# Kernel tuning notes

Measured on AMD Instinct MI355X. Metric: run time of the kernel, lower is better.

Reference implementation:

```python
import jax, jax.numpy as jnp
import numpy as np

# Dimensions (match init_kwargs / input_specs)
B, C, H, W = 16, 96, 224, 224
COUT = 96
PH, PW = 16, 16          # patch_size (== patch_stride, non-overlapping)
KH, KW = 3, 3            # patch_kernel and output_kernel
PAD = 1                  # padding
GH, GW = H // PH, W // PW
P = GH * GW              # num_patches = 196


def setup_inputs() -> dict:
    key = jax.random.key(0)
    k1, k2, k3 = jax.random.split(key, 3)
    x = jax.random.normal(k1, (B, C, H, W), dtype=jnp.float32)
    # kaiming-normal-ish init scales (fan_in over trailing dims, as torch does)
    pf = jax.random.normal(k2, (C, P, 1, KH, KW), dtype=jnp.float32) * np.float32(np.sqrt(2.0 / (P * KH * KW)))
    of = jax.random.normal(k3, (COUT, C, KH, KW), dtype=jnp.float32) * np.float32(np.sqrt(2.0 / (C * KH * KW)))
    return {"x": x, "patch_filters": pf, "output_filters": of}


def _self_conv2d(x, patch_filters):
    """Locally-connected per-patch depthwise conv.

    x: (B, C, H, W); patch_filters: (C, P, 1, KH, KW).
    Each of the P non-overlapping PHxPW patches of each channel is convolved
    with its own KHxKW kernel (padding=PAD, stride=1), then patches are
    reassembled into the full (B, C, H, W) map.
    """
    # (B, C, GH, PH, GW, PW) -> (B, C, GH, GW, PH, PW) -> (B, C*P, PH, PW)
    xp = x.reshape(B, C, GH, PH, GW, PW).transpose(0, 1, 2, 4, 3, 5).reshape(B, C * P, PH, PW)
    k = patch_filters.reshape(C * P, 1, KH, KW)
    y = jax.lax.conv_general_dilated(
        xp, k,
        window_strides=(1, 1),
        padding=[(PAD, PAD), (PAD, PAD)],
        feature_group_count=C * P,
        dimension_numbers=("NCHW", "OIHW", "NCHW"),
    )  # (B, C*P, PH, PW) since 3x3 conv with pad 1 preserves size
    return y.reshape(B, C, GH, GW, PH, PW).transpose(0, 1, 2, 4, 3, 5).reshape(B, C, H, W)


def reference(x, patch_filters, output_filters):
    # input already at (max_input_height, max_input_width) -> F.pad is a no-op
    sa = _self_conv2d(x, patch_filters)
    out = jax.lax.conv_general_dilated(
        sa, output_filters,
        window_strides=(1, 1),
        padding=[(PAD, PAD), (PAD, PAD)],
        dimension_numbers=("NCHW", "OIHW", "NCHW"),
    )  # (B, COUT, H, W)
    return jax.nn.gelu(out, approximate=False)  # torch nn.GELU() = exact erf gelu
```

## Files before the change

kernel.cpp:

```cpp
#include <hip/hip_runtime.h>
#include <hip/hip_bf16.h>

#define B_    16
#define C_    96
#define H_    224
#define W_    224
#define COUT_ 96
#define GH_   14
#define GW_   14
#define P_    196
#define HW_   (H_*W_)
#define NCH_  12

#define AS1 __attribute__((address_space(1)))
#define AS3 __attribute__((address_space(3)))

typedef __attribute__((ext_vector_type(8))) unsigned short ushort8;
typedef __attribute__((ext_vector_type(8))) short        short8;
typedef __attribute__((ext_vector_type(4))) float        f32x4;

__device__ __forceinline__ unsigned short f2bf(float f) {
    union { __hip_bfloat16 h; unsigned short u; } cv;
    cv.h = __float2bfloat16(f);
    return cv.u;
}

__global__ __launch_bounds__(256) void prep_ofb(const float* __restrict__ of,
                                                unsigned short* __restrict__ ofb3,
                                                unsigned short* __restrict__ zp) {
    if (blockIdx.x == 0 && threadIdx.x < 128) zp[threadIdx.x] = 0;
    int e = blockIdx.x * 256 + threadIdx.x;
    if (e < 82944) {
        int j    = e & 7;
        int l    = (e >> 3) & 63;
        int ni   = (e >> 9) % 6;
        int cs   = (e / 3072) % 3;
        int tap  = e / 9216;
        int cout = ni * 16 + (l & 15);
        int c    = cs * 32 + (l >> 4) * 8 + j;
        ofb3[e] = f2bf(of[((size_t)cout * 96 + c) * 9 + tap]);
    }
}

__global__ __launch_bounds__(256) void sa_kernel(const float* __restrict__ x,
                                                 const float* __restrict__ pf,
                                                 unsigned short* __restrict__ sa) {
    int bid   = blockIdx.x;
    int patch = bid % P_;
    int b     = bid / P_;
    int gh = patch / GW_, gw = patch % GW_;
    int t  = threadIdx.x;
    int py = t >> 4, px = t & 15;
    int y  = gh * 16 + py, xx = gw * 16 + px;

    __shared__ float xs[2][8][256];

    const float* xp0 = x + (size_t)b * C_ * HW_ + (size_t)y * W_ + xx;

    float lf[8];
    #pragma unroll
    for (int ch = 0; ch < 8; ++ch) lf[ch] = xp0[(size_t)ch * HW_];

    for (int cc = 0; cc < NCH_; ++cc) {
        int buf = cc & 1;
        #pragma unroll
        for (int ch = 0; ch < 8; ++ch) xs[buf][ch][t] = lf[ch];
        __syncthreads();
        if (cc < NCH_ - 1) {
            #pragma unroll
            for (int ch = 0; ch < 8; ++ch)
                lf[ch] = xp0[(size_t)((cc + 1) * 8 + ch) * HW_];
        }

        ushort8 v;
        #pragma unroll
        for (int ch = 0; ch < 8; ++ch) {
            const float* wgt = pf + ((size_t)(cc * 8 + ch) * P_ + patch) * 9;
            float a = 0.f;
            #pragma unroll
            for (int dy = -1; dy <= 1; ++dy) {
                int yy = py + dy;
                if ((unsigned)yy < 16u) {
                    #pragma unroll
                    for (int dx = -1; dx <= 1; ++dx) {
                        int xq = px + dx;
                        if ((unsigned)xq < 16u)
                            a = fmaf(xs[buf][ch][yy * 16 + xq],
                                     wgt[(dy + 1) * 3 + (dx + 1)], a);
                    }
                }
            }
            v[ch] = f2bf(a);
        }
        *(ushort8*)&sa[(((size_t)(b * NCH_ + cc) * H_ + y) * W_ + xx) * 8] = v;
    }
}

__global__ __launch_bounds__(256, 3) void conv2_mfma(const unsigned short* __restrict__ sa,
                                                     const unsigned short* __restrict__ ofb3,
                                                     const unsigned short* __restrict__ zp,
                                                     float* __restrict__ out) {
    int bid0 = blockIdx.x;
    int bid  = (bid0 % 8) * (6272 / 8) + bid0 / 8;
    int half = bid & 1;
    int pid  = bid >> 1;
    int patch = pid % P_;
    int b     = pid / P_;
    int gh = patch / GW_, gw = patch % GW_;
    int y0 = gh * 16 + half * 8, x0 = gw * 16;

    int t = threadIdx.x;
    int w = t >> 6, l = t & 63;
    int wm = w & 1, wn = w >> 1;
    int mrow = l & 15, kgrp = l >> 4;

    __shared__ ushort8 at8[2304];

    #pragma unroll
    for (int i = 0; i < 9; ++i) {
        int v = t + i * 256;
        const unsigned short* src = zp;
        if (v < 2160) {
            int ccl = v / 180, hpx = v - ccl * 180;
            int gy = y0 - 1 + hpx / 18, gx = x0 - 1 + hpx % 18;
            if ((unsigned)gy < (unsigned)H_ && (unsigned)gx < (unsigned)W_)
                src = &sa[(((size_t)(b * NCH_ + ccl) * H_ + gy) * W_ + gx) * 8];
        }
        __builtin_amdgcn_global_load_lds((const AS1 unsigned int*)src,
                                         (AS3 unsigned int*)&at8[v], 16, 0, 0);
    }

    f32x4 acc[4][3];
    #pragma unroll
    for (int mi = 0; mi < 4; ++mi)
        #pragma unroll
        for (int ni = 0; ni < 3; ++ni)
            acc[mi][ni] = (f32x4)0.f;

    __syncthreads();

    const unsigned short* at = (const unsigned short*)at8;

    short8 bfA[3], bfB[3];
    auto LOADBF = [&](short8* dst, int T) {
        const unsigned short* p = ofb3 + (size_t)(T / 3) * 9216 + (T % 3) * 3072
                                  + (wn * 3) * 512 + l * 8;
        #pragma unroll
        for (int nj = 0; nj < 3; ++nj)
            dst[nj] = *(const short8*)&p[nj * 512];
    };

    LOADBF(bfA, 0);
    #pragma unroll
    for (int T = 0; T < 27; ++T) {
        short8* cur = (T & 1) ? bfB : bfA;
        short8* nxt = (T & 1) ? bfA : bfB;
        if (T + 1 < 27) LOADBF(nxt, T + 1);
        __builtin_amdgcn_sched_barrier(0);

        int tap = T / 3, cs = T % 3;
        int ky = tap / 3, kx = tap % 3;
        #pragma unroll
        for (int mi = 0; mi < 4; ++mi) {
            short8 af = *(const short8*)&at[((cs * 4 + kgrp) * 180
                                            + (wm * 4 + mi + ky) * 18
                                            + kx + mrow) * 8];
            #pragma unroll
            for (int nj = 0; nj < 3; ++nj)
                acc[mi][nj] = __builtin_amdgcn_mfma_f32_16x16x32_bf16(
                    af, cur[nj], acc[mi][nj], 0, 0, 0);
        }
    }

    #pragma unroll
    for (int mi = 0; mi < 4; ++mi) {
        int gy = y0 + wm * 4 + mi;
        #pragma unroll
        for (int nj = 0; nj < 3; ++nj) {
            int cout = (wn * 3 + nj) * 16 + mrow;
            f32x4 gv;
            #pragma unroll
            for (int j = 0; j < 4; ++j) {
                float vv = acc[mi][nj][j];
                gv[j] = 0.5f * vv * (1.0f + erff(vv * 0.70710678118f));
            }
            *(f32x4*)&out[((size_t)b * COUT_ + cout) * HW_ + (size_t)gy * W_ +
                          x0 + kgrp * 4] = gv;
        }
    }
}

extern "C" void kernel_launch(void* const* d_in, const int* in_sizes, int n_in,
                              void* d_out, int out_size, void* d_ws, size_t ws_size,
                              hipStream_t stream) {
    const float* x  = (const float*)d_in[0];
    const float* pf = (const float*)d_in[1];
    const float* of = (const float*)d_in[2];
    float* out = (float*)d_out;

    unsigned short* sa   = (unsigned short*)d_ws;
    unsigned short* ofb3 = (unsigned short*)((char*)d_ws + 154140672);
    unsigned short* zp   = (unsigned short*)((char*)d_ws + 154306560);

    prep_ofb<<<324, 256, 0, stream>>>(of, ofb3, zp);
    sa_kernel<<<B_ * P_, 256, 0, stream>>>(x, pf, sa);
    conv2_mfma<<<B_ * P_ * 2, 256, 0, stream>>>(sa, ofb3, zp, out);
}
```

Before: 382.2 us.

## Merge weight prep into sa kernel, pad LDS pitch, double-buffer A fragments

Folds the output-filter bf16 conversion into the self-conv kernel as extra blocks, which removes one launch. Pads the per-channel-chunk LDS pitch from 180 to 181 entries so A-fragment reads from different k-groups hit different LDS banks. Software-pipelines the A-fragment LDS reads one step ahead, alongside the existing B-fragment prefetch, so MFMAs overlap with LDS latency. The cost is more VGPRs for the extra fragment buffers, which may reduce occupancy under the 3-wave launch bound.

New measurement: 363.0 us. 5.0% less time.

```diff
diff --git a/kernel.cpp b/kernel.cpp
--- a/kernel.cpp
+++ b/kernel.cpp
@@ -11,6 +11,7 @@
 #define P_    196
 #define HW_   (H_*W_)
 #define NCH_  12
+#define APITCH 181
 
 #define AS1 __attribute__((address_space(1)))
 #define AS3 __attribute__((address_space(3)))
@@ -25,27 +26,31 @@
     return cv.u;
 }
 
-__global__ __launch_bounds__(256) void prep_ofb(const float* __restrict__ of,
-                                                unsigned short* __restrict__ ofb3,
-                                                unsigned short* __restrict__ zp) {
-    if (blockIdx.x == 0 && threadIdx.x < 128) zp[threadIdx.x] = 0;
-    int e = blockIdx.x * 256 + threadIdx.x;
-    if (e < 82944) {
-        int j    = e & 7;
-        int l    = (e >> 3) & 63;
-        int ni   = (e >> 9) % 6;
-        int cs   = (e / 3072) % 3;
-        int tap  = e / 9216;
-        int cout = ni * 16 + (l & 15);
-        int c    = cs * 32 + (l >> 4) * 8 + j;
-        ofb3[e] = f2bf(of[((size_t)cout * 96 + c) * 9 + tap]);
-    }
-}
-
-__global__ __launch_bounds__(256) void sa_kernel(const float* __restrict__ x,
-                                                 const float* __restrict__ pf,
-                                                 unsigned short* __restrict__ sa) {
-    int bid   = blockIdx.x;
+__global__ __launch_bounds__(256) void sa_prep_kernel(const float* __restrict__ x,
+                                                      const float* __restrict__ pf,
+                                                      unsigned short* __restrict__ sa,
+                                                      const float* __restrict__ of,
+                                                      unsigned short* __restrict__ ofb3,
+                                                      unsigned short* __restrict__ zp) {
+    int bid = blockIdx.x;
+
+    if (bid >= B_ * P_) {
+        int pb = bid - B_ * P_;
+        if (pb == 0 && threadIdx.x < 128) zp[threadIdx.x] = 0;
+        int e = pb * 256 + threadIdx.x;
+        if (e < 82944) {
+            int j    = e & 7;
+            int l    = (e >> 3) & 63;
+            int ni   = (e >> 9) % 6;
+            int cs   = (e / 3072) % 3;
+            int tap  = e / 9216;
+            int cout = ni * 16 + (l & 15);
+            int c    = cs * 32 + (l >> 4) * 8 + j;
+            ofb3[e] = f2bf(of[((size_t)cout * 96 + c) * 9 + tap]);
+        }
+        return;
+    }
+
     int patch = bid % P_;
     int b     = bid / P_;
     int gh = patch / GW_, gw = patch % GW_;
@@ -120,11 +125,13 @@
     for (int i = 0; i < 9; ++i) {
         int v = t + i * 256;
         const unsigned short* src = zp;
-        if (v < 2160) {
-            int ccl = v / 180, hpx = v - ccl * 180;
-            int gy = y0 - 1 + hpx / 18, gx = x0 - 1 + hpx % 18;
-            if ((unsigned)gy < (unsigned)H_ && (unsigned)gx < (unsigned)W_)
-                src = &sa[(((size_t)(b * NCH_ + ccl) * H_ + gy) * W_ + gx) * 8];
+        if (v < 2172) {
+            int ccl = v / APITCH, hpx = v - ccl * APITCH;
+            if (hpx < 180) {
+                int gy = y0 - 1 + hpx / 18, gx = x0 - 1 + hpx % 18;
+                if ((unsigned)gy < (unsigned)H_ && (unsigned)gx < (unsigned)W_)
+                    src = &sa[(((size_t)(b * NCH_ + ccl) * H_ + gy) * W_ + gx) * 8];
+            }
         }
         __builtin_amdgcn_global_load_lds((const AS1 unsigned int*)src,
                                          (AS3 unsigned int*)&at8[v], 16, 0, 0);
@@ -141,7 +148,7 @@
 
     const unsigned short* at = (const unsigned short*)at8;
 
-    short8 bfA[3], bfB[3];
+    short8 bfA[3], bfB[3], afA[4], afB[4];
     auto LOADBF = [&](short8* dst, int T) {
         const unsigned short* p = ofb3 + (size_t)(T / 3) * 9216 + (T % 3) * 3072
                                   + (wn * 3) * 512 + l * 8;
@@ -149,27 +156,36 @@
         for (int nj = 0; nj < 3; ++nj)
             dst[nj] = *(const short8*)&p[nj * 512];
     };
-
-    LOADBF(bfA, 0);
-    #pragma unroll
-    for (int T = 0; T < 27; ++T) {
-        short8* cur = (T & 1) ? bfB : bfA;
-        short8* nxt = (T & 1) ? bfA : bfB;
-        if (T + 1 < 27) LOADBF(nxt, T + 1);
-        __builtin_amdgcn_sched_barrier(0);
-
+    auto LOADAF = [&](short8* dst, int T) {
         int tap = T / 3, cs = T % 3;
         int ky = tap / 3, kx = tap % 3;
         #pragma unroll
-        for (int mi = 0; mi < 4; ++mi) {
-            short8 af = *(const short8*)&at[((cs * 4 + kgrp) * 180
-                                            + (wm * 4 + mi + ky) * 18
-                                            + kx + mrow) * 8];
+        for (int mi = 0; mi < 4; ++mi)
+            dst[mi] = *(const short8*)&at[((cs * 4 + kgrp) * APITCH
+                                          + (wm * 4 + mi + ky) * 18
+                                          + kx + mrow) * 8];
+    };
+
+    LOADBF(bfA, 0);
+    LOADAF(afA, 0);
+    #pragma unroll
+    for (int T = 0; T < 27; ++T) {
+        short8* bcur = (T & 1) ? bfB : bfA;
+        short8* bnxt = (T & 1) ? bfA : bfB;
+        short8* acur = (T & 1) ? afB : afA;
+        short8* anxt = (T & 1) ? afA : afB;
+        if (T + 1 < 27) {
+            LOADBF(bnxt, T + 1);
+            LOADAF(anxt, T + 1);
+        }
+        __builtin_amdgcn_sched_barrier(0);
+
+        #pragma unroll
+        for (int mi = 0; mi < 4; ++mi)
             #pragma unroll
             for (int nj = 0; nj < 3; ++nj)
                 acc[mi][nj] = __builtin_amdgcn_mfma_f32_16x16x32_bf16(
-                    af, cur[nj], acc[mi][nj], 0, 0, 0);
-        }
+                    acur[mi], bcur[nj], acc[mi][nj], 0, 0, 0);
     }
 
     #pragma unroll
@@ -202,7 +218,6 @@
     unsigned short* ofb3 = (unsigned short*)((char*)d_ws + 154140672);
     unsigned short* zp   = (unsigned short*)((char*)d_ws + 154306560);
 
-    prep_ofb<<<324, 256, 0, stream>>>(of, ofb3, zp);
-    sa_kernel<<<B_ * P_, 256, 0, stream>>>(x, pf, sa);
+    sa_prep_kernel<<<B_ * P_ + 324, 256, 0, stream>>>(x, pf, sa, of, ofb3, zp);
     conv2_mfma<<<B_ * P_ * 2, 256, 0, stream>>>(sa, ofb3, zp, out);
 }
```
